# Kernel optimization log

Measured on AMD Instinct MI355X. Metric: run time of the kernel, lower is better.

## Reference

```python
import jax, jax.numpy as jnp
import numpy as np


def get_grid_index(init_grid_size, map_size):
    # nearest-neighbor 'interpolation' of flat indices, matching F.interpolate(mode='nearest')
    H_init, W_init = init_grid_size
    H, W = map_size
    # torch nearest: src index = floor(dst * scale), scale = src/dst
    rows = jnp.floor(jnp.arange(H_init) * (H / H_init)).astype(jnp.int32)
    cols = jnp.floor(jnp.arange(W_init) * (W / W_init)).astype(jnp.int32)
    idx = rows[:, None] * W + cols[None, :]
    return idx.reshape(-1)  # [N_init]


def _map2token(feature_map, idx_token, N, H_init, W_init):
    B, C, H, W = feature_map.shape
    N_init = H_init * W_init
    idx_hw = get_grid_index((H_init, W_init), (H, W))  # [N_init]
    # gather per-grid feature values: fm_flat[b, idx_hw] -> [B, N_init, C]
    fm = feature_map.transpose(0, 2, 3, 1).reshape(B, H * W, C)
    src = fm[:, idx_hw, :]  # [B, N_init, C]
    # scatter-add into tokens with counts
    def scatter_b(src_b, idx_b):
        num = jnp.zeros((N, C), src_b.dtype).at[idx_b].add(src_b)
        cnt = jnp.zeros((N,), src_b.dtype).at[idx_b].add(1.0)
        return num / (cnt + 1e-6)[:, None]
    return jax.vmap(scatter_b)(src, idx_token)  # [B, N, C]


def _token2map(x, idx_token, H, W, H_init, W_init):
    B, N, C = x.shape
    N_init = H_init * W_init
    idx_hw = get_grid_index((H_init, W_init), (H, W))  # [N_init]
    # each initial grid point contributes token x[b, idx_token[b,i]] to map cell idx_hw[i]
    def scatter_b(x_b, idx_tok_b):
        src = x_b[idx_tok_b]  # [N_init, C]
        num = jnp.zeros((H * W, C), x_b.dtype).at[idx_hw].add(src)
        cnt = jnp.zeros((H * W,), x_b.dtype).at[idx_hw].add(1.0)
        return num / (cnt + 1e-6)[:, None]
    out = jax.vmap(scatter_b)(x, idx_token)  # [B, H*W, C]
    return out.reshape(B, H, W, C).transpose(0, 3, 1, 2)


def setup_inputs() -> dict:
    key = jax.random.key(0)
    k1, k2, k3 = jax.random.split(key, 3)
    B, C, H, W = 8, 256, 56, 56
    N = 784
    H_init = W_init = 56
    N_init = H_init * W_init
    feature_map = jax.random.normal(k1, (B, C, H, W), dtype=jnp.float32)
    x = jax.random.normal(k2, (B, N, C), dtype=jnp.float32)
    idx_token = jax.random.randint(k3, (B, N_init), 0, N)
    return {"feature_map": feature_map, "x": x, "idx_token": idx_token,
            "token_num": N, "map_H": H, "map_W": W, "init_H": H_init, "init_W": W_init}


def reference(feature_map, x, idx_token, token_num, map_H, map_W, init_H, init_W):
    tokens = _map2token(feature_map, idx_token, token_num, init_H, init_W)
    fmap = _token2map(x, idx_token, map_H, map_W, init_H, init_W)
    return tokens, fmap
```

## Files before the change

kernel.cpp:

```cpp
#include <hip/hip_runtime.h>

#define BATCH 8
#define CCH   256
#define HWSZ  3136
#define NTOK  784
#define NINIT 3136

#define TOK_BLOCKS  (BATCH * (CCH / 4))
#define FMAP_BLOCKS (BATCH * (HWSZ / 64))
#define GRID        (TOK_BLOCKS + FMAP_BLOCKS)

#define SMEM_BYTES 47040

__global__ __launch_bounds__(1024, 8) void fused_kernel(
    const float* __restrict__ fm,
    const float* __restrict__ x,
    const int*   __restrict__ idx,
    float*       __restrict__ tokens,
    float*       __restrict__ fmap)
{
    __shared__ __align__(16) char smem[SMEM_BYTES];
    const int bid = blockIdx.x;
    const int tid = threadIdx.x;

    if (bid < TOK_BLOCKS) {
        float* plane = (float*)smem;
        int*   idx_s = (int*)(smem + 25088);
        float* acc   = (float*)(smem + 37632);
        int*   cnt_s = (int*)(smem + 43904);

        const int b  = bid & 7;
        const int c0 = (bid >> 3) * 4;

        if (tid < NINIT / 4)
            ((int4*)idx_s)[tid] = ((const int4*)(idx + b * NINIT))[tid];
        if (tid < NTOK) cnt_s[tid] = 0;
        __syncthreads();

        for (int i = tid; i < NINIT; i += 1024)
            atomicAdd(&cnt_s[idx_s[i]], 1);

        #pragma unroll
        for (int pair = 0; pair < 2; ++pair) {
            const int c = c0 + pair * 2;
            if (tid < NTOK) { acc[tid] = 0.f; acc[NTOK + tid] = 0.f; }
            const float4* src = (const float4*)(fm + ((size_t)(b * CCH + c)) * HWSZ);
            float4* pl4 = (float4*)plane;
            for (int v = tid; v < 2 * HWSZ / 4; v += 1024) pl4[v] = src[v];
            __syncthreads();

            for (int i = tid; i < NINIT; i += 1024) {
                const int n = idx_s[i];
                atomicAdd(&acc[n],        plane[i]);
                atomicAdd(&acc[NTOK + n], plane[HWSZ + i]);
            }
            __syncthreads();

            if (tid < NTOK) {
                const float s = 1.0f / ((float)cnt_s[tid] + 1e-6f);
                float2 w2;
                w2.x = acc[tid] * s;
                w2.y = acc[NTOK + tid] * s;
                *(float2*)&tokens[((size_t)(b * NTOK + tid)) * CCH + c] = w2;
            }
            __syncthreads();
        }
    } else {
        float (*tile)[65] = (float (*)[65])smem;
        int* ns = (int*)(smem + 64 * 65 * 4);

        int t = bid - TOK_BLOCKS;
        const int b  = t & 7;
        const int it = t >> 3;
        const int i0 = it * 64;

        const int lane = tid & 63;
        const int w    = tid >> 6;
        const int q    = tid & 15;
        const int r    = tid >> 4;

        if (tid < 64) ns[tid] = idx[b * NINIT + i0 + tid];
        __syncthreads();

        const float invc = 1.0f / (1.0f + 1e-6f);
        float* outb = fmap + (size_t)b * CCH * HWSZ;
        for (int ct = 0; ct < 4; ++ct) {
            const int c0 = ct * 64;
            const float4 v = *(const float4*)&x[((size_t)(b * NTOK + ns[r])) * CCH + c0 + q * 4];
            tile[r][q * 4 + 0] = v.x;
            tile[r][q * 4 + 1] = v.y;
            tile[r][q * 4 + 2] = v.z;
            tile[r][q * 4 + 3] = v.w;
            __syncthreads();
            #pragma unroll
            for (int cc = w; cc < 64; cc += 16)
                outb[(size_t)(c0 + cc) * HWSZ + i0 + lane] = tile[lane][cc] * invc;
            __syncthreads();
        }
    }
}

extern "C" void kernel_launch(void* const* d_in, const int* in_sizes, int n_in,
                              void* d_out, int out_size, void* d_ws, size_t ws_size,
                              hipStream_t stream) {
    const float* fm  = (const float*)d_in[0];
    const float* x   = (const float*)d_in[1];
    const int*   idx = (const int*)d_in[2];

    float* tokens = (float*)d_out;
    float* fmap   = (float*)d_out + (size_t)BATCH * NTOK * CCH;

    fused_kernel<<<GRID, 1024, 0, stream>>>(fm, x, idx, tokens, fmap);
}
```

Baseline: 128.2 us.

## Split fused kernel into separate tokens and fmap kernels with register prefetch

Splits the single fused kernel into two launches: a tokens kernel and a fmap kernel. The tokens kernel now handles 8 channels per block. It loads feature-map planes straight into registers, prefetching the next pair while atomically scattering the current pair into double-buffered shared accumulators, so the shared-memory staging plane goes away. The fmap kernel loads two 64-channel tiles per sync phase to halve the barriers. The cost is an extra launch, fewer token blocks, and the loss of concurrency between the two halves within one grid.

```diff
diff --git a/kernel.cpp b/kernel.cpp
--- a/kernel.cpp
+++ b/kernel.cpp
@@ -6,97 +6,134 @@
 #define NTOK  784
 #define NINIT 3136
 
-#define TOK_BLOCKS  (BATCH * (CCH / 4))
-#define FMAP_BLOCKS (BATCH * (HWSZ / 64))
-#define GRID        (TOK_BLOCKS + FMAP_BLOCKS)
+__global__ __launch_bounds__(1024) void tokens_kernel(
+    const float* __restrict__ fm,
+    const int*   __restrict__ idx,
+    float*       __restrict__ tokens)
+{
+    __shared__ int   idx_s[NINIT];
+    __shared__ int   cnt_s[NTOK];
+    __shared__ float acc[2][2 * NTOK];
 
-#define SMEM_BYTES 47040
+    const int tid = threadIdx.x;
+    const int b   = blockIdx.x & 7;
+    const int c0  = (blockIdx.x >> 3) * 8;
 
-__global__ __launch_bounds__(1024, 8) void fused_kernel(
-    const float* __restrict__ fm,
+    const float* fmb = fm + ((size_t)b * CCH + c0) * HWSZ;
+
+    if (tid < NINIT / 4)
+        ((int4*)idx_s)[tid] = ((const int4*)(idx + b * NINIT))[tid];
+    if (tid < NTOK) {
+        cnt_s[tid] = 0;
+        acc[0][tid] = 0.f; acc[0][NTOK + tid] = 0.f;
+        acc[1][tid] = 0.f; acc[1][NTOK + tid] = 0.f;
+    }
+    const int v0 = tid, v1 = tid + 1024;
+    const bool has1 = (v1 < 2 * HWSZ / 4);
+    float4 Ra0, Ra1, Rb0, Rb1;
+    {
+        const float4* s0 = (const float4*)(fmb + 0 * 2 * HWSZ);
+        Ra0 = s0[v0]; if (has1) Ra1 = s0[v1];
+        const float4* s1 = (const float4*)(fmb + 1 * 2 * HWSZ);
+        Rb0 = s1[v0]; if (has1) Rb1 = s1[v1];
+    }
+    __syncthreads();
+
+    for (int i = tid; i < NINIT; i += 1024)
+        atomicAdd(&cnt_s[idx_s[i]], 1);
+
+#define SCATTER(X0, X1, buf)                                                  \
+    {                                                                         \
+        _Pragma("unroll")                                                     \
+        for (int t = 0; t < 4; ++t) {                                         \
+            const int j  = 4 * tid + t;                                       \
+            const int ch = (j >= HWSZ) ? 1 : 0;                               \
+            const int i  = j - ch * HWSZ;                                     \
+            atomicAdd(&acc[buf][ch * NTOK + idx_s[i]], ((const float*)&X0)[t]);\
+        }                                                                     \
+        if (has1) {                                                           \
+            _Pragma("unroll")                                                 \
+            for (int t = 0; t < 4; ++t) {                                     \
+                const int i = 4 * tid + 960 + t;                              \
+                atomicAdd(&acc[buf][NTOK + idx_s[i]], ((const float*)&X1)[t]);\
+            }                                                                 \
+        }                                                                     \
+    }
+
+#define WRITEOUT(p, buf)                                                      \
+    if (tid < NTOK) {                                                         \
+        const float s = 1.0f / ((float)cnt_s[tid] + 1e-6f);                   \
+        float2 w2;                                                            \
+        w2.x = acc[buf][tid] * s;                                             \
+        w2.y = acc[buf][NTOK + tid] * s;                                      \
+        *(float2*)&tokens[((size_t)(b * NTOK + tid)) * CCH + c0 + 2 * (p)] = w2;\
+        acc[buf][tid] = 0.f; acc[buf][NTOK + tid] = 0.f;                      \
+    }
+
+    SCATTER(Ra0, Ra1, 0);
+    { const float4* s = (const float4*)(fmb + 2 * 2 * HWSZ);
+      Ra0 = s[v0]; if (has1) Ra1 = s[v1]; }
+    __syncthreads();
+    WRITEOUT(0, 0);
+    SCATTER(Rb0, Rb1, 1);
+    { const float4* s = (const float4*)(fmb + 3 * 2 * HWSZ);
+      Rb0 = s[v0]; if (has1) Rb1 = s[v1]; }
+    __syncthreads();
+    WRITEOUT(1, 1);
+    SCATTER(Ra0, Ra1, 0);
+    __syncthreads();
+    WRITEOUT(2, 0);
+    SCATTER(Rb0, Rb1, 1);
+    __syncthreads();
+    WRITEOUT(3, 1);
+#undef SCATTER
+#undef WRITEOUT
+}
+
+__global__ __launch_bounds__(1024) void fmap_kernel(
     const float* __restrict__ x,
     const int*   __restrict__ idx,
-    float*       __restrict__ tokens,
     float*       __restrict__ fmap)
 {
-    __shared__ __align__(16) char smem[SMEM_BYTES];
-    const int bid = blockIdx.x;
+    __shared__ float tile[2][64][65];
+    __shared__ int   ns[64];
+
     const int tid = threadIdx.x;
+    const int b   = blockIdx.x & 7;
+    const int it  = blockIdx.x >> 3;
+    const int i0  = it * 64;
 
-    if (bid < TOK_BLOCKS) {
-        float* plane = (float*)smem;
-        int*   idx_s = (int*)(smem + 25088);
-        float* acc   = (float*)(smem + 37632);
-        int*   cnt_s = (int*)(smem + 43904);
+    const int lane = tid & 63;
+    const int w    = tid >> 6;
+    const int q    = tid & 15;
+    const int r    = tid >> 4;
 
-        const int b  = bid & 7;
-        const int c0 = (bid >> 3) * 4;
+    if (tid < 64) ns[tid] = idx[b * NINIT + i0 + tid];
+    __syncthreads();
 
-        if (tid < NINIT / 4)
-            ((int4*)idx_s)[tid] = ((const int4*)(idx + b * NINIT))[tid];
-        if (tid < NTOK) cnt_s[tid] = 0;
+    const float* xrow = x + ((size_t)b * NTOK + ns[r]) * CCH;
+    const float invc  = 1.0f / (1.0f + 1e-6f);
+    float* outb = fmap + (size_t)b * CCH * HWSZ;
+
+    #pragma unroll
+    for (int h = 0; h < 2; ++h) {
+        const float4 va = *(const float4*)&xrow[(2 * h + 0) * 64 + q * 4];
+        const float4 vb = *(const float4*)&xrow[(2 * h + 1) * 64 + q * 4];
+        tile[0][r][q * 4 + 0] = va.x;  tile[0][r][q * 4 + 1] = va.y;
+        tile[0][r][q * 4 + 2] = va.z;  tile[0][r][q * 4 + 3] = va.w;
+        tile[1][r][q * 4 + 0] = vb.x;  tile[1][r][q * 4 + 1] = vb.y;
+        tile[1][r][q * 4 + 2] = vb.z;  tile[1][r][q * 4 + 3] = vb.w;
         __syncthreads();
-
-        for (int i = tid; i < NINIT; i += 1024)
-            atomicAdd(&cnt_s[idx_s[i]], 1);
-
         #pragma unroll
-        for (int pair = 0; pair < 2; ++pair) {
-            const int c = c0 + pair * 2;
-            if (tid < NTOK) { acc[tid] = 0.f; acc[NTOK + tid] = 0.f; }
-            const float4* src = (const float4*)(fm + ((size_t)(b * CCH + c)) * HWSZ);
-            float4* pl4 = (float4*)plane;
-            for (int v = tid; v < 2 * HWSZ / 4; v += 1024) pl4[v] = src[v];
-            __syncthreads();
-
-            for (int i = tid; i < NINIT; i += 1024) {
-                const int n = idx_s[i];
-                atomicAdd(&acc[n],        plane[i]);
-                atomicAdd(&acc[NTOK + n], plane[HWSZ + i]);
+        for (int k = 0; k < 2; ++k) {
+            const int c0 = (2 * h + k) * 64;
+            #pragma unroll
+            for (int cc0 = 0; cc0 < 64; cc0 += 16) {
+                const int cc = cc0 + w;
+                outb[(size_t)(c0 + cc) * HWSZ + i0 + lane] = tile[k][lane][cc] * invc;
             }
-            __syncthreads();
-
-            if (tid < NTOK) {
-                const float s = 1.0f / ((float)cnt_s[tid] + 1e-6f);
-                float2 w2;
-                w2.x = acc[tid] * s;
-                w2.y = acc[NTOK + tid] * s;
-                *(float2*)&tokens[((size_t)(b * NTOK + tid)) * CCH + c] = w2;
-            }
-            __syncthreads();
         }
-    } else {
-        float (*tile)[65] = (float (*)[65])smem;
-        int* ns = (int*)(smem + 64 * 65 * 4);
-
-        int t = bid - TOK_BLOCKS;
-        const int b  = t & 7;
-        const int it = t >> 3;
-        const int i0 = it * 64;
-
-        const int lane = tid & 63;
-        const int w    = tid >> 6;
-        const int q    = tid & 15;
-        const int r    = tid >> 4;
-
-        if (tid < 64) ns[tid] = idx[b * NINIT + i0 + tid];
         __syncthreads();
-
-        const float invc = 1.0f / (1.0f + 1e-6f);
-        float* outb = fmap + (size_t)b * CCH * HWSZ;
-        for (int ct = 0; ct < 4; ++ct) {
-            const int c0 = ct * 64;
-            const float4 v = *(const float4*)&x[((size_t)(b * NTOK + ns[r])) * CCH + c0 + q * 4];
-            tile[r][q * 4 + 0] = v.x;
-            tile[r][q * 4 + 1] = v.y;
-            tile[r][q * 4 + 2] = v.z;
-            tile[r][q * 4 + 3] = v.w;
-            __syncthreads();
-            #pragma unroll
-            for (int cc = w; cc < 64; cc += 16)
-                outb[(size_t)(c0 + cc) * HWSZ + i0 + lane] = tile[lane][cc] * invc;
-            __syncthreads();
-        }
     }
 }
 
@@ -110,5 +147,6 @@
     float* tokens = (float*)d_out;
     float* fmap   = (float*)d_out + (size_t)BATCH * NTOK * CCH;
 
-    fused_kernel<<<GRID, 1024, 0, stream>>>(fm, x, idx, tokens, fmap);
+    tokens_kernel<<<BATCH * (CCH / 8), 1024, 0, stream>>>(fm, idx, tokens);
+    fmap_kernel<<<BATCH * (HWSZ / 64), 1024, 0, stream>>>(x, idx, fmap);
 }
```

Measured after the change: 127.2 us. Within noise of the previous version (-0.8%).
